# Optimization experiments

Measured on AMD Instinct MI355X. Metric: run time of the kernel, lower is better.

## Reference

```python
import jax, jax.numpy as jnp
import numpy as np

B, S, HID = 2, 2048, 2048
H, KH, D = 16, 4, 128  # heads, kv heads, head_dim
N_REP = H // KH
SCALE = D ** -0.5


def rotate_half(x):
    x1, x2 = x[..., : D // 2], x[..., D // 2:]
    return jnp.concatenate((-x2, x1), axis=-1)


def setup_inputs() -> dict:
    key = jax.random.key(0)
    ks = jax.random.split(key, 6)
    hidden_states = jax.random.normal(ks[0], (B, S, HID), jnp.float32)
    # standard RoPE cos/sin tables, shape [B, S, D]
    inv_freq = 1.0 / (10000.0 ** (np.arange(0, D, 2, dtype=np.float32) / D))
    pos = np.arange(S, dtype=np.float32)
    freqs = np.outer(pos, inv_freq)            # [S, D/2]
    emb = np.concatenate([freqs, freqs], -1)   # [S, D]
    cos = jnp.broadcast_to(jnp.cos(emb), (B, S, D)).astype(jnp.float32)
    sin = jnp.broadcast_to(jnp.sin(emb), (B, S, D)).astype(jnp.float32)
    # additive causal mask [1, 1, S, S]
    neg = jnp.finfo(jnp.float32).min
    causal = jnp.triu(jnp.full((S, S), neg, jnp.float32), k=1)
    attention_mask = causal[None, None]
    std = 0.02
    wq = jax.random.normal(ks[1], (HID, H * D), jnp.float32) * std
    wk = jax.random.normal(ks[2], (HID, KH * D), jnp.float32) * std
    wv = jax.random.normal(ks[3], (HID, KH * D), jnp.float32) * std
    wo = jax.random.normal(ks[4], (H * D, HID), jnp.float32) * std
    return {"hidden_states": hidden_states, "cos": cos, "sin": sin,
            "attention_mask": attention_mask, "wq": wq, "wk": wk, "wv": wv, "wo": wo}


def reference(hidden_states, cos, sin, attention_mask, wq, wk, wv, wo):
    b, s, _ = hidden_states.shape
    q = (hidden_states @ wq).reshape(b, s, H, D).transpose(0, 2, 1, 3)   # [b,H,s,d]
    k = (hidden_states @ wk).reshape(b, s, KH, D).transpose(0, 2, 1, 3)  # [b,KH,s,d]
    v = (hidden_states @ wv).reshape(b, s, KH, D).transpose(0, 2, 1, 3)
    c = cos[:, None, :, :]  # [b,1,s,d] broadcast over heads
    sn = sin[:, None, :, :]
    q = q * c + rotate_half(q) * sn
    k = k * c + rotate_half(k) * sn
    # GQA: repeat KV heads
    k = jnp.repeat(k, N_REP, axis=1)  # [b,H,s,d]
    v = jnp.repeat(v, N_REP, axis=1)
    scores = jnp.einsum('bhqd,bhkd->bhqk', q, k) * SCALE + attention_mask
    probs = jax.nn.softmax(scores, axis=-1)
    attn = jnp.einsum('bhqk,bhkd->bhqd', probs, v)
    attn = attn.transpose(0, 2, 1, 3).reshape(b, s, H * D)
    return attn @ wo
```

## Files before the change

kernel.cpp:

```cpp
#include <hip/hip_runtime.h>
#include <stdint.h>

#define Bc   2
#define Sc   2048
#define HIDc 2048
#define Hc   16
#define KHc  4
#define Dc   128
#define HDc  2048
#define KHDc 512
#define QKVS 3072
#define SCALE2c 0.12751744657f
#define M0c 6.0f
#define N_ITEMS2 768

typedef _Float16 f16;
typedef _Float16 f16x2 __attribute__((ext_vector_type(2)));
typedef _Float16 f16x4 __attribute__((ext_vector_type(4)));
typedef _Float16 f16x8 __attribute__((ext_vector_type(8)));
typedef float    f32x4 __attribute__((ext_vector_type(4)));

__device__ __forceinline__ void gl_lds16(const void* g, void* l) {
  __builtin_amdgcn_global_load_lds(
      (const __attribute__((address_space(1))) unsigned int*)g,
      (__attribute__((address_space(3))) unsigned int*)l, 16, 0, 0);
}

__global__ __launch_bounds__(256) void conv_hs(const float* __restrict__ in,
                                               f16* __restrict__ out,
                                               int* __restrict__ ctr) {
  if (blockIdx.x == 0 && threadIdx.x == 0) *ctr = 0;
  int i = (blockIdx.x * 256 + threadIdx.x) * 4;
  float4 v = *(const float4*)&in[i];
  f16x4 o; o[0] = (f16)v.x; o[1] = (f16)v.y; o[2] = (f16)v.z; o[3] = (f16)v.w;
  *(f16x4*)&out[i] = o;
}

__global__ __launch_bounds__(256) void trw_all(const float* __restrict__ wq,
                                               const float* __restrict__ wk,
                                               const float* __restrict__ wv,
                                               const float* __restrict__ wo,
                                               f16* __restrict__ wqkvT,
                                               f16* __restrict__ woT) {
  const int z = blockIdx.z;
  const float* in; f16* out; int C, rowOff;
  if (z == 0)      { in = wq; out = wqkvT; C = 2048; rowOff = 0; }
  else if (z == 1) { in = wk; out = wqkvT; C = 512;  rowOff = 2048; }
  else if (z == 2) { in = wv; out = wqkvT; C = 512;  rowOff = 2560; }
  else             { in = wo; out = woT;   C = 2048; rowOff = 0; }
  if (blockIdx.x * 64 >= C) return;
  __shared__ float Ld[64 * 65];
  const int tid = threadIdx.x;
  const int r0 = blockIdx.y * 64, c0 = blockIdx.x * 64;
#pragma unroll
  for (int p = 0; p < 4; ++p) {
    int idx = p * 256 + tid;
    int r = idx >> 4, c4 = (idx & 15) * 4;
    float4 v = *(const float4*)&in[(size_t)(r0 + r) * C + c0 + c4];
    Ld[r * 65 + c4 + 0] = v.x; Ld[r * 65 + c4 + 1] = v.y;
    Ld[r * 65 + c4 + 2] = v.z; Ld[r * 65 + c4 + 3] = v.w;
  }
  __syncthreads();
#pragma unroll
  for (int p = 0; p < 4; ++p) {
    int idx = p * 256 + tid;
    int oc = idx >> 4, m4 = (idx & 15) * 4;
    f16x4 o;
#pragma unroll
    for (int i = 0; i < 4; ++i) o[i] = (f16)Ld[(m4 + i) * 65 + oc];
    *(f16x4*)&out[(size_t)(rowOff + c0 + oc) * 2048 + r0 + m4] = o;
  }
}

__global__ __launch_bounds__(256) void rope8(f16* __restrict__ x,
                                             const float* __restrict__ cb,
                                             const float* __restrict__ sb) {
  int bid = blockIdx.x;
  int colbase, idx, h, row;
  if (bid < 2048) { idx = bid * 256 + threadIdx.x; colbase = 0;    h = (idx >> 3) & 15; row = idx >> 7; }
  else            { idx = (bid - 2048) * 256 + threadIdx.x; colbase = 2048; h = (idx >> 3) & 3;  row = idx >> 5; }
  const int d0 = (idx & 7) * 8;
  f16* p = x + (size_t)row * QKVS + colbase + h * 128 + d0;
  f16x8 x1 = *(const f16x8*)p;
  f16x8 x2 = *(const f16x8*)(p + 64);
  const float* cp = cb + (size_t)row * 128 + d0;
  const float* sp = sb + (size_t)row * 128 + d0;
  float4 c0 = *(const float4*)cp, c1 = *(const float4*)(cp + 4);
  float4 s0 = *(const float4*)sp, s1 = *(const float4*)(sp + 4);
  float cc[8] = {c0.x, c0.y, c0.z, c0.w, c1.x, c1.y, c1.z, c1.w};
  float ss[8] = {s0.x, s0.y, s0.z, s0.w, s1.x, s1.y, s1.z, s1.w};
  f16x8 y1, y2;
#pragma unroll
  for (int i = 0; i < 8; ++i) {
    float a = (float)x1[i], b = (float)x2[i];
    y1[i] = (f16)(a * cc[i] - b * ss[i]);
    y2[i] = (f16)(b * cc[i] + a * ss[i]);
  }
  *(f16x8*)p = y1;
  *(f16x8*)(p + 64) = y2;
}

__global__ __launch_bounds__(256) void v_tr(const f16* __restrict__ QKV,
                                            f16* __restrict__ Vt) {
  __shared__ f16 Ld[64 * 78];
  const int tid = threadIdx.x;
  const int s0 = blockIdx.x * 64, d0 = blockIdx.y * 64;
  const int b = blockIdx.z >> 2, kh = blockIdx.z & 3;
#pragma unroll
  for (int p = 0; p < 2; ++p) {
    int idx = p * 256 + tid;
    int sl = idx >> 3, dc8 = (idx & 7) * 8;
    f16x8 v = *(const f16x8*)&QKV[(size_t)(b * Sc + s0 + sl) * QKVS + 2560 + kh * 128 + d0 + dc8];
#pragma unroll
    for (int i = 0; i < 4; ++i) {
      f16x2 w; w[0] = v[2 * i]; w[1] = v[2 * i + 1];
      *(f16x2*)&Ld[sl * 78 + dc8 + 2 * i] = w;
    }
  }
  __syncthreads();
  {
    int dr = (tid >> 3) * 2, sc8 = (tid & 7) * 8;
    f16x8 r0v, r1v;
#pragma unroll
    for (int j = 0; j < 8; ++j) {
      f16x2 w = *(const f16x2*)&Ld[(sc8 + j) * 78 + dr];
      r0v[j] = w[0]; r1v[j] = w[1];
    }
    size_t obase = ((size_t)(b * KHc + kh) * 128 + d0 + dr) * Sc + s0 + sc8;
    *(f16x8*)&Vt[obase]      = r0v;
    *(f16x8*)&Vt[obase + Sc] = r1v;
  }
}

template<int NREP, int CF16>
__global__ __launch_bounds__(512, 4) void gemm128(const f16* __restrict__ A,
                                                  const f16* __restrict__ Bt,
                                                  void* __restrict__ Cout,
                                                  int K, int cstride) {
  __shared__ f16 Al[2][8192];
  __shared__ f16 Bl[2][NREP * 4096];
  const int tid  = threadIdx.x;
  const int lane = tid & 63, wave = tid >> 6;
  const int quad = lane >> 4, l16 = lane & 15;
  const int wm = wave >> 2, wn = wave & 3;
  const int m0 = blockIdx.y * 128, n0 = blockIdx.x * (NREP * 64);
  f32x4 acc[4][NREP] = {};

  auto stage = [&](int buf, int k0) {
#pragma unroll
    for (int p = 0; p < 2; ++p) {
      gl_lds16(&A[(size_t)(m0 + wave * 16 + l16) * K + k0 + p * 32 + quad * 8],
               &Al[buf][(wave * 2 + p) * 512]);
    }
#pragma unroll
    for (int p = 0; p < NREP; ++p) {
      const int gb = wave * NREP + p;
      const int gi = gb >> 1, kh2 = gb & 1;
      gl_lds16(&Bt[(size_t)(n0 + gi * 16 + l16) * K + k0 + kh2 * 32 + quad * 8],
               &Bl[buf][gb * 512]);
    }
  };

  stage(0, 0);
  const int NT = K >> 6;
  for (int t = 0; t < NT; ++t) {
    const int cur = t & 1;
    __syncthreads();
    if (t + 1 < NT) stage(cur ^ 1, (t + 1) * 64);

    f16x8 bf[NREP][2];
#pragma unroll
    for (int j = 0; j < NREP; ++j)
#pragma unroll
      for (int ks = 0; ks < 2; ++ks)
        bf[j][ks] = *(const f16x8*)&Bl[cur][((wn * NREP + j) * 2 + ks) * 512 + quad * 128 + l16 * 8];
    f16x8 af[4][2];
#pragma unroll
    for (int i = 0; i < 4; ++i)
#pragma unroll
      for (int ks = 0; ks < 2; ++ks)
        af[i][ks] = *(const f16x8*)&Al[cur][((wm * 4 + i) * 2 + ks) * 512 + quad * 128 + l16 * 8];
    __builtin_amdgcn_s_setprio(1);
#pragma unroll
    for (int ks = 0; ks < 2; ++ks)
#pragma unroll
      for (int i = 0; i < 4; ++i)
#pragma unroll
        for (int j = 0; j < NREP; ++j)
          acc[i][j] = __builtin_amdgcn_mfma_f32_16x16x32_f16(
              af[i][ks], bf[j][ks], acc[i][j], 0, 0, 0);
    __builtin_amdgcn_s_setprio(0);
  }

  const int rbase = m0 + wm * 64;
  const int cbase = n0 + wn * NREP * 16;
#pragma unroll
  for (int mi = 0; mi < 4; ++mi)
#pragma unroll
    for (int j = 0; j < NREP; ++j)
#pragma unroll
      for (int r = 0; r < 4; ++r) {
        size_t idx = (size_t)(rbase + mi * 16 + quad * 4 + r) * cstride + cbase + j * 16 + l16;
        if (CF16) ((f16*)Cout)[idx]   = (f16)acc[mi][j][r];
        else      ((float*)Cout)[idx] = acc[mi][j][r];
      }
}

__global__ __launch_bounds__(512, 4) void attn_v8(const f16* __restrict__ QKV,
                                                  const f16* __restrict__ Vt,
                                                  f16* __restrict__ Ob,
                                                  f16* __restrict__ Opart,
                                                  float2* __restrict__ ML,
                                                  int* __restrict__ ctr) {
  __shared__ f16 Kl[2][8192];
  __shared__ f16 Vl[2][8192];
  __shared__ f16 Ps[8 * 512];
  __shared__ int item_s;
  const int tid  = threadIdx.x;
  const int lane = tid & 63, wave = tid >> 6;
  const int quad = lane >> 4, l16 = lane & 15;
  const int qsel = wave >> 2, wv = wave & 3;

  f16x8 ones_f;
#pragma unroll
  for (int i = 0; i < 8; ++i) ones_f[i] = (l16 == 0) ? (f16)1.0f : (f16)0.0f;

  for (;;) {
    if (tid == 0) item_s = atomicAdd(ctr, 1);
    __syncthreads();
    const int item = item_s;
    if (item >= N_ITEMS2) break;

    int p, bh, k0t, k1t, hf = -1;
    if (item < 640) {
      int base = 0, c = 16;
#pragma unroll 1
      for (; c >= 9; --c) {
        int sz = (c & 1) ? 64 : 96;
        if (item < base + sz) break;
        base += sz;
      }
      int off = item - base;
      if (off < 64) {
        p = c - 1; hf = off >> 5; bh = off & 31;
        int hn = p + 1;
        k0t = hf ? hn : 0; k1t = hf ? 2 * p + 2 : hn;
      } else {
        p = (c >> 1) - 1; bh = off - 64; k0t = 0; k1t = 2 * p + 2;
      }
    } else {
      int off = item - 640;
      p = 3 - (off >> 5); bh = off & 31; k0t = 0; k1t = 2 * p + 2;
    }
    const int b = bh >> 4, h = bh & 15, kh = h >> 2;
    const int qt = 2 * p + qsel;
    const int qbase = qt * 64 + wv * 16;

    f16x8 qf[4];
    {
      const f16* qp = QKV + (size_t)(b * Sc + qbase + l16) * QKVS + h * 128 + quad * 8;
#pragma unroll
      for (int c = 0; c < 4; ++c) qf[c] = *(const f16x8*)(qp + c * 32);
    }
    f32x4 ls = {};
    f32x4 o[8] = {};

    auto stageKV = [&](int kt, int buf) {
#pragma unroll
      for (int p2 = 0; p2 < 2; ++p2) {
        const int g = wave * 2 + p2;
        gl_lds16(&QKV[(size_t)(b * Sc + kt * 64 + (g >> 2) * 16 + l16) * QKVS + 2048 + kh * 128 + (g & 3) * 32 + quad * 8],
                 &Kl[buf][g * 512]);
      }
#pragma unroll
      for (int p2 = 0; p2 < 2; ++p2) {
        const int g = wave * 2 + p2;
        gl_lds16(&Vt[(size_t)((b * KHc + kh) * 128 + (g >> 1) * 16 + l16) * Sc + kt * 64 + (g & 1) * 32 + quad * 8],
                 &Vl[buf][g * 512]);
      }
    };

    stageKV(k0t, 0);
    stageKV(k0t + 1, 1);

    for (int kt = k0t; kt < k1t; ++kt) {
      const int cur = (kt - k0t) & 1;
      if (kt + 1 < k1t) { asm volatile("s_waitcnt vmcnt(4)" ::: "memory"); }
      else              { asm volatile("s_waitcnt vmcnt(0)" ::: "memory"); }
      __builtin_amdgcn_sched_barrier(0);
      __builtin_amdgcn_s_barrier();
      __builtin_amdgcn_sched_barrier(0);

      if (kt <= qt) {
        __builtin_amdgcn_s_setprio(1);
        f32x4 s4[4] = {};
#pragma unroll
        for (int kc = 0; kc < 2; ++kc)
#pragma unroll
          for (int c = 0; c < 4; ++c) {
            f16x8 ka = *(const f16x8*)&Kl[cur][(((kc * 2 + 0) * 4 + c) * 4 + quad) * 128 + l16 * 8];
            f16x8 kb = *(const f16x8*)&Kl[cur][(((kc * 2 + 1) * 4 + c) * 4 + quad) * 128 + l16 * 8];
            s4[kc * 2 + 0] = __builtin_amdgcn_mfma_f32_16x16x32_f16(qf[c], ka, s4[kc * 2 + 0], 0, 0, 0);
            s4[kc * 2 + 1] = __builtin_amdgcn_mfma_f32_16x16x32_f16(qf[c], kb, s4[kc * 2 + 1], 0, 0, 0);
          }
        __builtin_amdgcn_s_setprio(0);

        const bool diag = (kt == qt);
        const int cb = kt * 64 + l16;
        const int wb  = wave * 512 + (l16 & 7);
        const int rhi = l16 >> 3;
        float e2[4], e3[4];
#pragma unroll
        for (int r = 0; r < 4; ++r) {
          float v0 = fmaf(s4[0][r], SCALE2c, -M0c);
          float v1 = fmaf(s4[1][r], SCALE2c, -M0c);
          float v2 = fmaf(s4[2][r], SCALE2c, -M0c);
          float v3 = fmaf(s4[3][r], SCALE2c, -M0c);
          if (diag) {
            const int qrow = qbase + quad * 4 + r;
            if (cb      > qrow) v0 = -1e30f;
            if (cb + 16 > qrow) v1 = -1e30f;
            if (cb + 32 > qrow) v2 = -1e30f;
            if (cb + 48 > qrow) v3 = -1e30f;
          }
          float p0 = exp2f(v0), p1 = exp2f(v1);
          e2[r] = exp2f(v2); e3[r] = exp2f(v3);
          const int rowoff = (quad * 4 + r) * 8;
          Ps[wb + (rhi + 0) * 128 + rowoff] = (f16)p0;
          Ps[wb + (rhi + 2) * 128 + rowoff] = (f16)p1;
        }

        {
          f16x8 pf = *(const f16x8*)&Ps[wave * 512 + quad * 128 + l16 * 8];
          __builtin_amdgcn_s_setprio(1);
          ls = __builtin_amdgcn_mfma_f32_16x16x32_f16(pf, ones_f, ls, 0, 0, 0);
#pragma unroll
          for (int dt = 0; dt < 8; ++dt) {
            f16x8 vf = *(const f16x8*)&Vl[cur][((dt * 2 + 0) * 4 + quad) * 128 + l16 * 8];
            o[dt] = __builtin_amdgcn_mfma_f32_16x16x32_f16(pf, vf, o[dt], 0, 0, 0);
          }
          __builtin_amdgcn_s_setprio(0);
        }
#pragma unroll
        for (int r = 0; r < 4; ++r) {
          const int rowoff = (quad * 4 + r) * 8;
          Ps[wb + (rhi + 0) * 128 + rowoff] = (f16)e2[r];
          Ps[wb + (rhi + 2) * 128 + rowoff] = (f16)e3[r];
        }
        {
          f16x8 pf = *(const f16x8*)&Ps[wave * 512 + quad * 128 + l16 * 8];
          __builtin_amdgcn_s_setprio(1);
          ls = __builtin_amdgcn_mfma_f32_16x16x32_f16(pf, ones_f, ls, 0, 0, 0);
#pragma unroll
          for (int dt = 0; dt < 8; ++dt) {
            f16x8 vf = *(const f16x8*)&Vl[cur][((dt * 2 + 1) * 4 + quad) * 128 + l16 * 8];
            o[dt] = __builtin_amdgcn_mfma_f32_16x16x32_f16(pf, vf, o[dt], 0, 0, 0);
          }
          __builtin_amdgcn_s_setprio(0);
        }
      }

      __builtin_amdgcn_sched_barrier(0);
      __builtin_amdgcn_s_barrier();
      __builtin_amdgcn_sched_barrier(0);
      if (kt + 2 < k1t) stageKV(kt + 2, cur);
    }

    float inv[4], lrow[4];
#pragma unroll
    for (int r = 0; r < 4; ++r) {
      lrow[r] = __shfl(ls[r], lane & 48);
      inv[r] = 1.0f / lrow[r];
    }
    const int rl = wv * 16 + quad * 4;
    if (hf < 0) {
#pragma unroll
      for (int dt = 0; dt < 8; ++dt)
#pragma unroll
        for (int r = 0; r < 4; ++r)
          Ob[(size_t)(b * Sc + qbase + quad * 4 + r) * HDc + h * 128 + dt * 16 + l16] =
              (f16)(o[dt][r] * inv[r]);
    } else {
      const int tile = (qt - 16) * 32 + bh;
      f16* op = Opart + ((size_t)tile * 2 + hf) * (64 * 128);
#pragma unroll
      for (int dt = 0; dt < 8; ++dt)
#pragma unroll
        for (int r = 0; r < 4; ++r)
          op[(rl + r) * 128 + dt * 16 + l16] = (f16)(o[dt][r] * inv[r]);
      if (l16 == 0) {
#pragma unroll
        for (int r = 0; r < 4; ++r) {
          float2 ml; ml.x = M0c; ml.y = lrow[r];
          ML[((size_t)tile * 2 + hf) * 64 + rl + r] = ml;
        }
      }
    }
  }
}

__global__ __launch_bounds__(256) void attn_merge(const f16* __restrict__ Opart,
                                                  const float2* __restrict__ ML,
                                                  f16* __restrict__ Ob) {
  const int tile = blockIdx.x;
  const int qt = 16 + (tile >> 5), bh = tile & 31;
  const int b = bh >> 4, h = bh & 15;
  const int tid = threadIdx.x;
  const int row = tid >> 2, c0 = (tid & 3) * 32;
  float2 ml1 = ML[(size_t)tile * 2 * 64 + row];
  float2 ml2 = ML[((size_t)tile * 2 + 1) * 64 + row];
  float m = fmaxf(ml1.x, ml2.x);
  float w1 = ml1.y * exp2f(ml1.x - m);
  float w2 = ml2.y * exp2f(ml2.x - m);
  float rinv = 1.0f / (w1 + w2);
  float a1 = w1 * rinv, a2 = w2 * rinv;
  const f16* o1 = Opart + (size_t)tile * 2 * (64 * 128) + row * 128 + c0;
  const f16* o2 = o1 + 64 * 128;
  f16* out = Ob + (size_t)(b * Sc + qt * 64 + row) * HDc + h * 128 + c0;
#pragma unroll
  for (int j = 0; j < 4; ++j) {
    f16x8 x1 = *(const f16x8*)(o1 + j * 8);
    f16x8 x2 = *(const f16x8*)(o2 + j * 8);
    f16x8 y;
#pragma unroll
    for (int i = 0; i < 8; ++i) y[i] = (f16)(a1 * (float)x1[i] + a2 * (float)x2[i]);
    *(f16x8*)(out + j * 8) = y;
  }
}

extern "C" void kernel_launch(void* const* d_in, const int* in_sizes, int n_in,
                              void* d_out, int out_size, void* d_ws, size_t ws_size,
                              hipStream_t stream) {
  (void)in_sizes; (void)n_in; (void)out_size; (void)ws_size;
  const float* hs   = (const float*)d_in[0];
  const float* cosb = (const float*)d_in[1];
  const float* sinb = (const float*)d_in[2];
  const float* wq = (const float*)d_in[4];
  const float* wk = (const float*)d_in[5];
  const float* wv = (const float*)d_in[6];
  const float* wo = (const float*)d_in[7];
  float* out = (float*)d_out;

  char* ws = (char*)d_ws;
  int*  ctr = (int*)ws;
  size_t off = 256;
  auto alloc = [&](size_t bytes) { char* p = ws + off; off += (bytes + 255) & ~(size_t)255; return p; };
  f16*  hsF   = (f16*)alloc((size_t)Bc * Sc * HIDc * 2);
  f16*  woT   = (f16*)alloc((size_t)HIDc * HDc * 2);
  f16*  QKVf  = (f16*)alloc((size_t)Bc * Sc * QKVS * 2);
  f16*  Vt_g  = (f16*)alloc((size_t)Bc * KHc * Dc * Sc * 2);
  f16*  wqkvT = (f16*)alloc((size_t)QKVS * HIDc * 2);
  f16*  Opart = wqkvT;
  {
    size_t opart_bytes = (size_t)512 * 2 * 64 * 128 * 2;
    size_t wqkvT_bytes = (size_t)QKVS * HIDc * 2;
    if (opart_bytes > wqkvT_bytes) off += opart_bytes - wqkvT_bytes;
  }
  float2* ML = (float2*)alloc((size_t)512 * 2 * 64 * sizeof(float2));
  f16*  attnF = hsF;

  conv_hs<<<8192, 256, 0, stream>>>(hs, hsF, ctr);
  trw_all<<<dim3(32, 32, 4), 256, 0, stream>>>(wq, wk, wv, wo, wqkvT, woT);

  gemm128<3, 1><<<dim3(16, 32), 512, 0, stream>>>(hsF, wqkvT, QKVf, 2048, QKVS);

  rope8<<<2560, 256, 0, stream>>>(QKVf, cosb, sinb);
  v_tr<<<dim3(32, 2, 8), 256, 0, stream>>>(QKVf, Vt_g);

  attn_v8<<<512, 512, 0, stream>>>(QKVf, Vt_g, attnF, Opart, ML, ctr);
  attn_merge<<<512, 256, 0, stream>>>(Opart, ML, attnF);

  gemm128<2, 0><<<dim3(16, 32), 512, 0, stream>>>(attnF, woT, out, 2048, 2048);
}
```

Baseline: 382.5 us.

## Enlarge GEMM M-tile to 256 and prefetch two stages ahead with vmcnt waits

The projection GEMM now computes 256-row tiles, so each wave holds 8×NREP accumulators and each B fragment is reused across twice as many A rows. Launch bounds drop to 2 blocks per SM and the grid halves. The pipeline now issues the next two k-stages up front and uses explicit vmcnt waits plus barriers, so a load stays in flight over two compute steps instead of one. The cost is more registers, more LDS and fewer blocks (256), which may underfill the 256 CUs and leaves no tail balancing.

```diff
diff --git a/kernel.cpp b/kernel.cpp
--- a/kernel.cpp
+++ b/kernel.cpp
@@ -133,24 +133,26 @@
 }
 
 template<int NREP, int CF16>
-__global__ __launch_bounds__(512, 4) void gemm128(const f16* __restrict__ A,
+__global__ __launch_bounds__(512, 2) void gemm8p2(const f16* __restrict__ A,
                                                   const f16* __restrict__ Bt,
                                                   void* __restrict__ Cout,
                                                   int K, int cstride) {
-  __shared__ f16 Al[2][8192];
+  __shared__ f16 Al[2][16384];
   __shared__ f16 Bl[2][NREP * 4096];
   const int tid  = threadIdx.x;
   const int lane = tid & 63, wave = tid >> 6;
   const int quad = lane >> 4, l16 = lane & 15;
   const int wm = wave >> 2, wn = wave & 3;
-  const int m0 = blockIdx.y * 128, n0 = blockIdx.x * (NREP * 64);
-  f32x4 acc[4][NREP] = {};
+  const int m0 = blockIdx.y * 256, n0 = blockIdx.x * (NREP * 64);
+  f32x4 acc[8][NREP] = {};
 
   auto stage = [&](int buf, int k0) {
 #pragma unroll
-    for (int p = 0; p < 2; ++p) {
-      gl_lds16(&A[(size_t)(m0 + wave * 16 + l16) * K + k0 + p * 32 + quad * 8],
-               &Al[buf][(wave * 2 + p) * 512]);
+    for (int p = 0; p < 4; ++p) {
+      const int g  = wave * 2 + (p >> 1);
+      const int kq = (p & 1) * 4 + quad;
+      gl_lds16(&A[(size_t)(m0 + g * 16 + l16) * K + k0 + kq * 8],
+               &Al[buf][(wave * 4 + p) * 512]);
     }
 #pragma unroll
     for (int p = 0; p < NREP; ++p) {
@@ -161,41 +163,57 @@
     }
   };
 
+  const int NT = K >> 6;
   stage(0, 0);
-  const int NT = K >> 6;
+  stage(1, 64);
   for (int t = 0; t < NT; ++t) {
     const int cur = t & 1;
-    __syncthreads();
-    if (t + 1 < NT) stage(cur ^ 1, (t + 1) * 64);
+    if (t + 1 < NT) {
+      if constexpr (NREP == 3) { asm volatile("s_waitcnt vmcnt(7)" ::: "memory"); }
+      else                     { asm volatile("s_waitcnt vmcnt(6)" ::: "memory"); }
+    } else {
+      asm volatile("s_waitcnt vmcnt(0)" ::: "memory");
+    }
+    __builtin_amdgcn_sched_barrier(0);
+    __builtin_amdgcn_s_barrier();
+    __builtin_amdgcn_sched_barrier(0);
 
     f16x8 bf[NREP][2];
 #pragma unroll
     for (int j = 0; j < NREP; ++j)
 #pragma unroll
       for (int ks = 0; ks < 2; ++ks)
-        bf[j][ks] = *(const f16x8*)&Bl[cur][((wn * NREP + j) * 2 + ks) * 512 + quad * 128 + l16 * 8];
-    f16x8 af[4][2];
-#pragma unroll
-    for (int i = 0; i < 4; ++i)
+        bf[j][ks] = *(const f16x8*)&Bl[cur][(((wn * NREP + j) * 8 + ks * 4 + quad) * 16 + l16) * 8];
+#pragma unroll
+    for (int mh = 0; mh < 2; ++mh) {
+      f16x8 af[4][2];
+#pragma unroll
+      for (int i = 0; i < 4; ++i)
+#pragma unroll
+        for (int ks = 0; ks < 2; ++ks)
+          af[i][ks] = *(const f16x8*)&Al[cur][(((wm * 8 + mh * 4 + i) * 8 + ks * 4 + quad) * 16 + l16) * 8];
+      __builtin_amdgcn_s_setprio(1);
 #pragma unroll
       for (int ks = 0; ks < 2; ++ks)
-        af[i][ks] = *(const f16x8*)&Al[cur][((wm * 4 + i) * 2 + ks) * 512 + quad * 128 + l16 * 8];
-    __builtin_amdgcn_s_setprio(1);
-#pragma unroll
-    for (int ks = 0; ks < 2; ++ks)
-#pragma unroll
-      for (int i = 0; i < 4; ++i)
-#pragma unroll
-        for (int j = 0; j < NREP; ++j)
-          acc[i][j] = __builtin_amdgcn_mfma_f32_16x16x32_f16(
-              af[i][ks], bf[j][ks], acc[i][j], 0, 0, 0);
-    __builtin_amdgcn_s_setprio(0);
-  }
-
-  const int rbase = m0 + wm * 64;
+#pragma unroll
+        for (int i = 0; i < 4; ++i)
+#pragma unroll
+          for (int j = 0; j < NREP; ++j)
+            acc[mh * 4 + i][j] = __builtin_amdgcn_mfma_f32_16x16x32_f16(
+                af[i][ks], bf[j][ks], acc[mh * 4 + i][j], 0, 0, 0);
+      __builtin_amdgcn_s_setprio(0);
+    }
+
+    __builtin_amdgcn_sched_barrier(0);
+    __builtin_amdgcn_s_barrier();
+    __builtin_amdgcn_sched_barrier(0);
+    if (t + 2 < NT) stage(cur, (t + 2) * 64);
+  }
+
+  const int rbase = m0 + wm * 128;
   const int cbase = n0 + wn * NREP * 16;
 #pragma unroll
-  for (int mi = 0; mi < 4; ++mi)
+  for (int mi = 0; mi < 8; ++mi)
 #pragma unroll
     for (int j = 0; j < NREP; ++j)
 #pragma unroll
@@ -462,7 +480,7 @@
   conv_hs<<<8192, 256, 0, stream>>>(hs, hsF, ctr);
   trw_all<<<dim3(32, 32, 4), 256, 0, stream>>>(wq, wk, wv, wo, wqkvT, woT);
 
-  gemm128<3, 1><<<dim3(16, 32), 512, 0, stream>>>(hsF, wqkvT, QKVf, 2048, QKVS);
+  gemm8p2<3, 1><<<dim3(16, 16), 512, 0, stream>>>(hsF, wqkvT, QKVf, 2048, QKVS);
 
   rope8<<<2560, 256, 0, stream>>>(QKVf, cosb, sinb);
   v_tr<<<dim3(32, 2, 8), 256, 0, stream>>>(QKVf, Vt_g);
@@ -470,5 +488,5 @@
   attn_v8<<<512, 512, 0, stream>>>(QKVf, Vt_g, attnF, Opart, ML, ctr);
   attn_merge<<<512, 256, 0, stream>>>(Opart, ML, attnF);
 
-  gemm128<2, 0><<<dim3(16, 32), 512, 0, stream>>>(attnF, woT, out, 2048, 2048);
-}
+  gemm8p2<2, 0><<<dim3(16, 16), 512, 0, stream>>>(attnF, woT, out, 2048, 2048);
+}
```

Measured after the change: 390.3 us. +2.1%, slower.
